# Performance work log

Measured on AMD Instinct MI355X. Metric: run time of the kernel, lower is better.

## Reference

```python
import jax, jax.numpy as jnp
import numpy as np

B, S, D, H, V, C = 4, 2048, 1024, 16, 32000, 10
FFN_DIM = 2 * D
HD = D // H
SCALE = float(np.sqrt(HD))


def _posenc(seq, d):
    pos = jnp.arange(seq, dtype=jnp.float32)[:, None]
    div = jnp.exp(jnp.arange(0, d, 2, dtype=jnp.float32) * (-np.log(10000.0) / d))
    pe = jnp.zeros((seq, d), dtype=jnp.float32)
    pe = pe.at[:, 0::2].set(jnp.sin(pos * div))
    pe = pe.at[:, 1::2].set(jnp.cos(pos * div))
    return pe


def _layernorm(x, g, b, eps=1e-5):
    mu = jnp.mean(x, axis=-1, keepdims=True)
    var = jnp.mean(jnp.square(x - mu), axis=-1, keepdims=True)
    return (x - mu) * jax.lax.rsqrt(var + eps) * g + b


def setup_inputs() -> dict:
    key = jax.random.key(0)
    ks = jax.random.split(key, 10)
    x_ids = jax.random.randint(ks[0], (B, S), 0, V, dtype=jnp.int64 if jax.config.jax_enable_x64 else jnp.int32)
    mask = jnp.ones((B, S), dtype=jnp.int32)
    emb = (jax.random.normal(ks[1], (V, D), jnp.float32) * 0.02).at[0].set(0.0)  # padding_idx=0
    qkv_w = jax.random.normal(ks[2], (3 * D, D), jnp.float32) * 0.02
    fc_w = jax.random.normal(ks[3], (D, D), jnp.float32) * 0.02
    fc_b = jnp.zeros((D,), jnp.float32)
    ln1_g = jnp.ones((D,), jnp.float32); ln1_b = jnp.zeros((D,), jnp.float32)
    ffn_w1 = jax.random.normal(ks[4], (FFN_DIM, D), jnp.float32) * 0.02
    ffn_b1 = jnp.zeros((FFN_DIM,), jnp.float32)
    ffn_w2 = jax.random.normal(ks[5], (D, FFN_DIM), jnp.float32) * 0.02
    ffn_b2 = jnp.zeros((D,), jnp.float32)
    ln2_g = jnp.ones((D,), jnp.float32); ln2_b = jnp.zeros((D,), jnp.float32)
    pr_w1 = jax.random.normal(ks[6], (D, D), jnp.float32) * 0.02
    pr_b1 = jnp.zeros((D,), jnp.float32)
    pr_w2 = jax.random.normal(ks[7], (C, D), jnp.float32) * 0.02
    pr_b2 = jnp.zeros((C,), jnp.float32)
    return dict(x_ids=x_ids, mask=mask, emb=emb, qkv_w=qkv_w, fc_w=fc_w, fc_b=fc_b,
                ln1_g=ln1_g, ln1_b=ln1_b, ffn_w1=ffn_w1, ffn_b1=ffn_b1,
                ffn_w2=ffn_w2, ffn_b2=ffn_b2, ln2_g=ln2_g, ln2_b=ln2_b,
                pr_w1=pr_w1, pr_b1=pr_b1, pr_w2=pr_w2, pr_b2=pr_b2)


def reference(x_ids, mask, emb, qkv_w, fc_w, fc_b, ln1_g, ln1_b,
              ffn_w1, ffn_b1, ffn_w2, ffn_b2, ln2_g, ln2_b,
              pr_w1, pr_b1, pr_w2, pr_b2):
    # embedding + absolute positional encoding
    x = emb[x_ids] + _posenc(S, D)  # [B,S,D]
    residual = x
    # multi-head attention (dropout is identity at eval)
    qkv = jnp.einsum('bsd,ed->bse', x, qkv_w)  # [B,S,3D]
    q, k, v = jnp.split(qkv, 3, axis=-1)
    q = q.reshape(B, S, H, HD)
    k = k.reshape(B, S, H, HD)
    v = v.reshape(B, S, H, HD)
    attn = jnp.einsum('bqhd,bkhd->bhqk', q, k) / SCALE  # [B,H,S,S]
    attn = jnp.where(mask[:, None, None, :] == 0, -jnp.inf, attn)
    attn = jax.nn.softmax(attn, axis=-1)
    o = jnp.einsum('bhqk,bkhd->bqhd', attn, v).reshape(B, S, D)
    o = jnp.einsum('bsd,ed->bse', o, fc_w) + fc_b
    x = _layernorm(o + residual, ln1_g, ln1_b)
    # FFN block (residual + LayerNorm inside)
    h = jax.nn.gelu(jnp.einsum('bsd,fd->bsf', x, ffn_w1) + ffn_b1, approximate=False)
    h = jnp.einsum('bsf,df->bsd', h, ffn_w2) + ffn_b2
    x = _layernorm(h + x, ln2_g, ln2_b)
    # masked max-pool over sequence
    x = jnp.where(mask[:, :, None] == 0, -jnp.inf, x).max(axis=1)  # [B,D]
    # prediction head
    h = jax.nn.gelu(x @ pr_w1.T + pr_b1, approximate=False)
    logits = h @ pr_w2.T + pr_b2  # [B,C]
    return logits
```

## Files before the change

kernel.cpp:

```cpp
#include <hip/hip_runtime.h>
#include <math.h>

#define B_   4
#define S_   2048
#define D_   1024
#define H_   16
#define HD_  64
#define C_   10
#define FFN_ 2048
#define M_   (B_ * S_)
#define D3_  (3 * D_)

typedef unsigned short u16;
typedef __bf16 bf16x8 __attribute__((ext_vector_type(8)));
typedef float  f32x4  __attribute__((ext_vector_type(4)));

#define EXPSCL 0.18033688011112042f

__device__ __forceinline__ u16 f2bf(float f) {
  union { float f; unsigned u; } x; x.f = f;
  unsigned r = x.u + 0x7fffu + ((x.u >> 16) & 1u);
  return (u16)(r >> 16);
}
__device__ __forceinline__ unsigned cvtpk(float lo, float hi) {
  unsigned r;
  asm("v_cvt_pk_bf16_f32 %0, %1, %2" : "=v"(r) : "v"(lo), "v"(hi));
  return r;
}
__device__ __forceinline__ float gelu_f(float x) {
  return 0.5f * x * (1.f + erff(x * 0.70710678118654752440f));
}
__device__ __forceinline__ void gload_lds16(const void* g, void* l) {
  __builtin_amdgcn_global_load_lds(
      (const __attribute__((address_space(1))) unsigned int*)g,
      (__attribute__((address_space(3))) unsigned int*)l, 16, 0, 0);
}
__device__ __forceinline__ bf16x8 ldsfrag(const u16* buf, int rowbase, int fr, int kb) {
  return *(const bf16x8*)&buf[(rowbase + fr) * 64 + ((kb ^ (fr & 7)) << 3)];
}

#define CV0 786432
#define CV1 262144
#define CV2 524288
#define CV3 524288
__global__ __launch_bounds__(256) void cvt4_kernel(const float* __restrict__ s0,
                                                   const float* __restrict__ s1,
                                                   const float* __restrict__ s2,
                                                   const float* __restrict__ s3,
                                                   u16* __restrict__ d0,
                                                   u16* __restrict__ d1,
                                                   u16* __restrict__ d2,
                                                   u16* __restrict__ d3) {
  int v = blockIdx.x * 256 + threadIdx.x;
  const float* s; u16* d;
  if (v < CV0) { s = s0; d = d0; }
  else if (v < CV0 + CV1) { s = s1; d = d1; v -= CV0; }
  else if (v < CV0 + CV1 + CV2) { s = s2; d = d2; v -= CV0 + CV1; }
  else { s = s3; d = d3; v -= CV0 + CV1 + CV2; }
  const int i = v * 4;
  f32x4 x = *(const f32x4*)&s[i];
  ushort4 o;
  o.x = f2bf(x[0]); o.y = f2bf(x[1]); o.z = f2bf(x[2]); o.w = f2bf(x[3]);
  *(ushort4*)&d[i] = o;
}

__global__ __launch_bounds__(256) void embed_kernel(const int* __restrict__ ids,
                                                    const float* __restrict__ emb,
                                                    float* __restrict__ resid,
                                                    u16* __restrict__ xb) {
  const int m  = blockIdx.x;
  const int s  = m & (S_ - 1);
  const int id = ids[m];
  const int d0 = threadIdx.x * 4;
#pragma unroll
  for (int k = 0; k < 4; ++k) {
    const int d   = d0 + k;
    const float e = emb[(size_t)id * D_ + d];
    const float fr  = expf((float)(d & ~1) * (-9.210340371976184f / 1024.0f));
    const float ang = (float)s * fr;
    const float pe  = (d & 1) ? cosf(ang) : sinf(ang);
    const float v   = e + pe;
    resid[(size_t)m * D_ + d] = v;
    xb[(size_t)m * D_ + d]    = f2bf(v);
  }
}

template <int BIAS, int GELU, int OUTBF, int QSCALE>
__global__ __launch_bounds__(256) void gemm_bt(const u16* __restrict__ A,
                                               const u16* __restrict__ W,
                                               const float* __restrict__ bias,
                                               float* __restrict__ outf,
                                               u16* __restrict__ outb,
                                               int M, int N, int K) {
  __shared__ u16 As[128 * 64];
  __shared__ u16 Bs[128 * 64];
  const int tid  = threadIdx.x;
  const int lane = tid & 63;
  const int w    = tid >> 6;
  const int bx   = blockIdx.x, by = blockIdx.y;
  const int l3   = lane >> 3;
  const int sb   = (lane & 7) ^ l3;
  const u16* Ag0 = A + (size_t)(by * 128 + w * 32 + l3) * K + sb * 8;
  const u16* Wg0 = W + (size_t)(bx * 128 + w * 32 + l3) * K + sb * 8;

  f32x4 acc[4][4] = {};
  const int wr  = (w & 1) * 64;
  const int wc  = (w >> 1) * 64;
  const int fr  = lane & 15;
  const int fq  = lane >> 4;

  for (int kt = 0; kt < K; kt += 64) {
#pragma unroll
    for (int c = 0; c < 4; ++c) {
      gload_lds16(Ag0 + (size_t)(c * 8) * K + kt, &As[(w * 32 + c * 8) * 64]);
      gload_lds16(Wg0 + (size_t)(c * 8) * K + kt, &Bs[(w * 32 + c * 8) * 64]);
    }
    __syncthreads();
#pragma unroll
    for (int ks = 0; ks < 2; ++ks) {
      const int kb = ks * 4 + fq;
      bf16x8 af[4], bfr[4];
#pragma unroll
      for (int i = 0; i < 4; ++i) af[i] = ldsfrag(As, wr + i * 16, fr, kb);
#pragma unroll
      for (int j = 0; j < 4; ++j) bfr[j] = ldsfrag(Bs, wc + j * 16, fr, kb);
#pragma unroll
      for (int i = 0; i < 4; ++i)
#pragma unroll
        for (int j = 0; j < 4; ++j)
          acc[i][j] = __builtin_amdgcn_mfma_f32_16x16x32_bf16(bfr[j], af[i], acc[i][j], 0, 0, 0);
    }
    __syncthreads();
  }

  const float qs = (QSCALE && bx < 8) ? EXPSCL : 1.f;
#pragma unroll
  for (int i = 0; i < 4; ++i) {
    const int m = by * 128 + wr + i * 16 + fr;
#pragma unroll
    for (int j = 0; j < 4; ++j) {
      const int nb = bx * 128 + wc + j * 16 + fq * 4;
      f32x4 v = acc[i][j];
      if (BIAS) v += *(const f32x4*)&bias[nb];
      if (GELU) {
        v[0] = gelu_f(v[0]); v[1] = gelu_f(v[1]);
        v[2] = gelu_f(v[2]); v[3] = gelu_f(v[3]);
      }
      if (QSCALE) v *= qs;
      if (OUTBF) {
        ushort4 pk;
        pk.x = f2bf(v[0]); pk.y = f2bf(v[1]); pk.z = f2bf(v[2]); pk.w = f2bf(v[3]);
        *(ushort4*)&outb[(size_t)m * N + nb] = pk;
      } else {
        *(f32x4*)&outf[(size_t)m * N + nb] = v;
      }
    }
  }
}

__global__ __launch_bounds__(256) void vtrans_kernel(const u16* __restrict__ qkv,
                                                     u16* __restrict__ vt) {
  __shared__ u16 t[64 * 65];
  const int tid = threadIdx.x;
  const int st = blockIdx.x, h = blockIdx.y, b = blockIdx.z;
  {
    const int r = tid & 63, cg = tid >> 6;
    const u16* src = qkv + (size_t)(b * S_ + st * 64 + r) * D3_ + 2 * D_ + h * 64 + cg * 16;
    union { uint4 q; u16 s[8]; } a, c;
    a.q = *(const uint4*)src;
    c.q = *(const uint4*)(src + 8);
    u16* dl = &t[r * 65 + cg * 16];
#pragma unroll
    for (int k = 0; k < 8; ++k) { dl[k] = a.s[k]; dl[8 + k] = c.s[k]; }
  }
  __syncthreads();
  const int d = tid >> 2, sq = tid & 3;
  union { uint4 q[2]; u16 s[16]; } o;
#pragma unroll
  for (int k = 0; k < 16; ++k) o.s[k] = t[(sq * 16 + k) * 65 + d];
  u16* dst = vt + ((size_t)((b * H_ + h) * 64 + d)) * S_ + st * 64 + sq * 16;
  *(uint4*)dst = o.q[0];
  *(uint4*)(dst + 8) = o.q[1];
}

__global__ __launch_bounds__(256) void attn_mfma_kernel(const u16* __restrict__ qkv,
                                                        const u16* __restrict__ vt,
                                                        const int* __restrict__ mask,
                                                        u16* __restrict__ attno) {
  __shared__ u16 Qs[128 * 64];
  __shared__ u16 Ks[64 * 64];
  __shared__ u16 Vts[64 * 64];
  __shared__ u16 Ps[4][16 * 64];
  int* allv_p = (int*)&Ps[0][0];
  const int tid = threadIdx.x, lane = tid & 63, w = tid >> 6;
  const int qt = blockIdx.x, h = blockIdx.y, b = blockIdx.z;
  const int l3 = lane >> 3;
  const int sb = (lane & 7) ^ l3;
  const int fr = lane & 15, fq = lane >> 4;

  {
    const u16* qbase = qkv + (size_t)(b * S_ + qt * 128 + w * 32) * D3_ + h * 64 + sb * 8;
#pragma unroll
    for (int c = 0; c < 4; ++c)
      gload_lds16(qbase + (size_t)(c * 8 + l3) * D3_, &Qs[(w * 32 + c * 8) * 64]);
  }
  if (tid == 0) *allv_p = 1;
  __syncthreads();
  {
    int mv = 1;
#pragma unroll
    for (int s0 = 0; s0 < 8; ++s0) mv &= (mask[b * S_ + s0 * 256 + tid] != 0);
    if (__ballot(mv != 0) != ~0ull) {
      if (lane == 0) atomicAnd(allv_p, 0);
    }
  }
  __syncthreads();
  const bool ALLV = (*allv_p != 0);

  float l_st[2] = {0.f, 0.f};
  f32x4 ot[4][2] = {};
  u16* PsW = Ps[w];

  for (int kt = 0; kt < S_ / 64; ++kt) {
    __syncthreads();
    {
      const u16* kbase = qkv + (size_t)(b * S_ + kt * 64 + w * 16) * D3_ + D_ + h * 64 + sb * 8;
      gload_lds16(kbase + (size_t)l3 * D3_, &Ks[(w * 16) * 64]);
      gload_lds16(kbase + (size_t)(8 + l3) * D3_, &Ks[(w * 16 + 8) * 64]);
      const u16* vbase = vt + ((size_t)((b * H_ + h) * 64 + w * 16)) * S_ + kt * 64 + sb * 8;
      gload_lds16(vbase + (size_t)l3 * S_, &Vts[(w * 16) * 64]);
      gload_lds16(vbase + (size_t)(8 + l3) * S_, &Vts[(w * 16 + 8) * 64]);
    }
    __syncthreads();

    f32x4 sf[4][2] = {};
#pragma unroll
    for (int ks = 0; ks < 2; ++ks) {
      const int kb = ks * 4 + fq;
      bf16x8 qf0 = ldsfrag(Qs, w * 32, fr, kb);
      bf16x8 qf1 = ldsfrag(Qs, w * 32 + 16, fr, kb);
      __builtin_amdgcn_s_setprio(1);
#pragma unroll
      for (int r4 = 0; r4 < 4; ++r4) {
        bf16x8 kf = ldsfrag(Ks, r4 * 16, fr, kb);
        sf[r4][0] = __builtin_amdgcn_mfma_f32_16x16x32_bf16(kf, qf0, sf[r4][0], 0, 0, 0);
        sf[r4][1] = __builtin_amdgcn_mfma_f32_16x16x32_bf16(kf, qf1, sf[r4][1], 0, 0, 0);
      }
      __builtin_amdgcn_s_setprio(0);
    }
    if (!ALLV) {
#pragma unroll
      for (int r4 = 0; r4 < 4; ++r4) {
        const int4 mm = *(const int4*)&mask[b * S_ + kt * 64 + r4 * 16 + fq * 4];
        f32x4 vb;
        vb[0] = mm.x ? 0.f : -1e30f;
        vb[1] = mm.y ? 0.f : -1e30f;
        vb[2] = mm.z ? 0.f : -1e30f;
        vb[3] = mm.w ? 0.f : -1e30f;
        sf[r4][0] += vb;
        sf[r4][1] += vb;
      }
    }

#pragma unroll
    for (int i = 0; i < 2; ++i) {
      u16* pw = PsW + fr * 64;
      float sum = l_st[i];
#pragma unroll
      for (int r4 = 0; r4 < 4; ++r4) {
        const float p0 = __builtin_exp2f(sf[r4][i][0]);
        const float p1 = __builtin_exp2f(sf[r4][i][1]);
        const float p2 = __builtin_exp2f(sf[r4][i][2]);
        const float p3 = __builtin_exp2f(sf[r4][i][3]);
        sum += (p0 + p1) + (p2 + p3);
        const int bk0 = 2 * r4 + (fq >> 1);
        const int off = ((bk0 ^ (fr & 7)) << 3) + ((fq & 1) << 2);
        uint2 pk; pk.x = cvtpk(p0, p1); pk.y = cvtpk(p2, p3);
        *(uint2*)&pw[off] = pk;
      }
      l_st[i] = sum;
      asm volatile("s_waitcnt lgkmcnt(0)" ::: "memory");

      bf16x8 pf0 = ldsfrag(PsW, 0, fr, fq);
      bf16x8 pf1 = ldsfrag(PsW, 0, fr, 4 + fq);
      __builtin_amdgcn_s_setprio(1);
#pragma unroll
      for (int db = 0; db < 4; ++db) {
        bf16x8 vf0 = ldsfrag(Vts, db * 16, fr, fq);
        bf16x8 vf1 = ldsfrag(Vts, db * 16, fr, 4 + fq);
        ot[db][i] = __builtin_amdgcn_mfma_f32_16x16x32_bf16(vf0, pf0, ot[db][i], 0, 0, 0);
        ot[db][i] = __builtin_amdgcn_mfma_f32_16x16x32_bf16(vf1, pf1, ot[db][i], 0, 0, 0);
      }
      __builtin_amdgcn_s_setprio(0);
    }
  }

#pragma unroll
  for (int i = 0; i < 2; ++i) {
    float l = l_st[i];
    l += __shfl_xor(l, 16);
    l += __shfl_xor(l, 32);
    const float inv = (l > 0.f) ? 1.f / l : 0.f;
    const int qrow = qt * 128 + w * 32 + i * 16 + fr;
    u16* dst = attno + (size_t)(b * S_ + qrow) * D_ + h * 64 + fq * 4;
#pragma unroll
    for (int db = 0; db < 4; ++db) {
      ushort4 pk;
      pk.x = f2bf(ot[db][i][0] * inv);
      pk.y = f2bf(ot[db][i][1] * inv);
      pk.z = f2bf(ot[db][i][2] * inv);
      pk.w = f2bf(ot[db][i][3] * inv);
      *(ushort4*)&dst[db * 16] = pk;
    }
  }
}

template <int WRITEB>
__global__ __launch_bounds__(256) void ln_kernel(const float* __restrict__ a,
                                                 const float* __restrict__ res,
                                                 const float* __restrict__ g,
                                                 const float* __restrict__ be,
                                                 float* __restrict__ outf,
                                                 u16* __restrict__ outb) {
  const int row = blockIdx.x, tid = threadIdx.x;
  const int lane = tid & 63, w = tid >> 6;
  const size_t base = (size_t)row * D_ + tid * 4;
  const f32x4 va = *(const f32x4*)(a + base);
  const f32x4 vr = *(const f32x4*)(res + base);
  const f32x4 v  = va + vr;
  float s = v[0] + v[1] + v[2] + v[3];
#pragma unroll
  for (int o = 32; o > 0; o >>= 1) s += __shfl_xor(s, o);
  __shared__ float red[8];
  if (lane == 0) red[w] = s;
  __syncthreads();
  const float mu = (red[0] + red[1] + red[2] + red[3]) * (1.f / D_);
  const f32x4 d = v - mu;
  float s2 = d[0] * d[0] + d[1] * d[1] + d[2] * d[2] + d[3] * d[3];
#pragma unroll
  for (int o = 32; o > 0; o >>= 1) s2 += __shfl_xor(s2, o);
  if (lane == 0) red[4 + w] = s2;
  __syncthreads();
  const float var = (red[4] + red[5] + red[6] + red[7]) * (1.f / D_);
  const float rs = rsqrtf(var + 1e-5f);
  f32x4 y;
#pragma unroll
  for (int k = 0; k < 4; ++k) {
    const int ch = tid * 4 + k;
    y[k] = d[k] * rs * g[ch] + be[ch];
  }
  *(f32x4*)&outf[base] = y;
  if (WRITEB) {
    ushort4 pk;
    pk.x = f2bf(y[0]); pk.y = f2bf(y[1]); pk.z = f2bf(y[2]); pk.w = f2bf(y[3]);
    *(ushort4*)&outb[base] = pk;
  }
}

__global__ __launch_bounds__(256) void pool_part_kernel(const float* __restrict__ x,
                                                        const int* __restrict__ mask,
                                                        float* __restrict__ part) {
  const int b = blockIdx.y, ch = blockIdx.x;
  const int d0 = threadIdx.x * 4;
  f32x4 acc = {-INFINITY, -INFINITY, -INFINITY, -INFINITY};
  for (int ss = 0; ss < 64; ++ss) {
    const int s = ch * 64 + ss;
    if (mask[b * S_ + s] != 0) {
      const f32x4 v = *(const f32x4*)&x[(size_t)(b * S_ + s) * D_ + d0];
      acc[0] = fmaxf(acc[0], v[0]);
      acc[1] = fmaxf(acc[1], v[1]);
      acc[2] = fmaxf(acc[2], v[2]);
      acc[3] = fmaxf(acc[3], v[3]);
    }
  }
  *(f32x4*)&part[(size_t)(b * 32 + ch) * D_ + d0] = acc;
}
__global__ __launch_bounds__(256) void pool_final_kernel(const float* __restrict__ part,
                                                         float* __restrict__ pooled) {
  const int b = blockIdx.x;
  const int d0 = threadIdx.x * 4;
  f32x4 acc = {-INFINITY, -INFINITY, -INFINITY, -INFINITY};
  for (int ch = 0; ch < 32; ++ch) {
    const f32x4 v = *(const f32x4*)&part[(size_t)(b * 32 + ch) * D_ + d0];
    acc[0] = fmaxf(acc[0], v[0]);
    acc[1] = fmaxf(acc[1], v[1]);
    acc[2] = fmaxf(acc[2], v[2]);
    acc[3] = fmaxf(acc[3], v[3]);
  }
  *(f32x4*)&pooled[(size_t)b * D_ + d0] = acc;
}

__global__ __launch_bounds__(256) void head1_kernel(const float* __restrict__ pooled,
                                                    const float* __restrict__ w,
                                                    const float* __restrict__ bias,
                                                    float* __restrict__ hh) {
  const int lane = threadIdx.x & 63;
  const int gw = blockIdx.x * 4 + (threadIdx.x >> 6);
  const int b = gw >> 10, n = gw & 1023;
  const float* p  = pooled + b * 1024;
  const float* wr = w + (size_t)n * 1024;
  float s = 0.f;
  for (int d = lane; d < 1024; d += 64) s += p[d] * wr[d];
#pragma unroll
  for (int off = 32; off > 0; off >>= 1) s += __shfl_xor(s, off);
  if (lane == 0) hh[b * 1024 + n] = gelu_f(s + bias[n]);
}
__global__ __launch_bounds__(256) void head2_kernel(const float* __restrict__ hh,
                                                    const float* __restrict__ w,
                                                    const float* __restrict__ bias,
                                                    float* __restrict__ out) {
  const int lane = threadIdx.x & 63;
  const int gw = blockIdx.x * 4 + (threadIdx.x >> 6);
  const int b = gw / 10, c = gw % 10;
  const float* p  = hh + b * 1024;
  const float* wr = w + (size_t)c * 1024;
  float s = 0.f;
  for (int d = lane; d < 1024; d += 64) s += p[d] * wr[d];
#pragma unroll
  for (int off = 32; off > 0; off >>= 1) s += __shfl_xor(s, off);
  if (lane == 0) out[b * 10 + c] = s + bias[c];
}

#define OFF_RESID  0UL
#define OFF_F1     33554432UL
#define OFF_XB     67108864UL
#define OFF_QKVB   83886080UL
#define OFF_ATTNO  134217728UL
#define OFF_WQKV   150994944UL
#define OFF_WFC    157286400UL
#define OFF_WF1    159383552UL
#define OFF_WF2    163577856UL
#define OFF_PART   167772160UL
#define OFF_POOLED 168296448UL
#define OFF_HH     168312832UL

extern "C" void kernel_launch(void* const* d_in, const int* in_sizes, int n_in,
                              void* d_out, int out_size, void* d_ws, size_t ws_size,
                              hipStream_t stream) {
  const int*   x_ids  = (const int*)d_in[0];
  const int*   mask   = (const int*)d_in[1];
  const float* emb    = (const float*)d_in[2];
  const float* qkv_w  = (const float*)d_in[3];
  const float* fc_w   = (const float*)d_in[4];
  const float* fc_b   = (const float*)d_in[5];
  const float* ln1_g  = (const float*)d_in[6];
  const float* ln1_b  = (const float*)d_in[7];
  const float* ffn_w1 = (const float*)d_in[8];
  const float* ffn_b1 = (const float*)d_in[9];
  const float* ffn_w2 = (const float*)d_in[10];
  const float* ffn_b2 = (const float*)d_in[11];
  const float* ln2_g  = (const float*)d_in[12];
  const float* ln2_b  = (const float*)d_in[13];
  const float* pr_w1  = (const float*)d_in[14];
  const float* pr_b1  = (const float*)d_in[15];
  const float* pr_w2  = (const float*)d_in[16];
  const float* pr_b2  = (const float*)d_in[17];
  float* out = (float*)d_out;
  char* ws = (char*)d_ws;

  float* resid  = (float*)(ws + OFF_RESID);
  float* f1     = (float*)(ws + OFF_F1);
  u16*   vtb    = (u16*)(ws + OFF_F1);
  u16*   xb     = (u16*)(ws + OFF_XB);
  u16*   qkvb   = (u16*)(ws + OFF_QKVB);
  u16*   hb     = (u16*)(ws + OFF_QKVB);
  u16*   attnob = (u16*)(ws + OFF_ATTNO);
  u16*   wqkvb  = (u16*)(ws + OFF_WQKV);
  u16*   wfcb   = (u16*)(ws + OFF_WFC);
  u16*   wf1b   = (u16*)(ws + OFF_WF1);
  u16*   wf2b   = (u16*)(ws + OFF_WF2);
  float* part   = (float*)(ws + OFF_PART);
  float* pooled = (float*)(ws + OFF_POOLED);
  float* hh     = (float*)(ws + OFF_HH);

  cvt4_kernel<<<8192, 256, 0, stream>>>(qkv_w, fc_w, ffn_w1, ffn_w2,
                                        wqkvb, wfcb, wf1b, wf2b);

  embed_kernel<<<M_, 256, 0, stream>>>(x_ids, emb, resid, xb);

  gemm_bt<0, 0, 1, 1><<<dim3(D3_ / 128, M_ / 128), 256, 0, stream>>>(
      xb, wqkvb, nullptr, nullptr, qkvb, M_, D3_, D_);

  vtrans_kernel<<<dim3(S_ / 64, H_, B_), 256, 0, stream>>>(qkvb, vtb);

  attn_mfma_kernel<<<dim3(S_ / 128, H_, B_), 256, 0, stream>>>(qkvb, vtb, mask, attnob);

  gemm_bt<1, 0, 0, 0><<<dim3(D_ / 128, M_ / 128), 256, 0, stream>>>(
      attnob, wfcb, fc_b, f1, nullptr, M_, D_, D_);

  ln_kernel<1><<<M_, 256, 0, stream>>>(f1, resid, ln1_g, ln1_b, resid, xb);

  gemm_bt<1, 1, 1, 0><<<dim3(FFN_ / 128, M_ / 128), 256, 0, stream>>>(
      xb, wf1b, ffn_b1, nullptr, hb, M_, FFN_, D_);

  gemm_bt<1, 0, 0, 0><<<dim3(D_ / 128, M_ / 128), 256, 0, stream>>>(
      hb, wf2b, ffn_b2, f1, nullptr, M_, D_, FFN_);

  ln_kernel<0><<<M_, 256, 0, stream>>>(f1, resid, ln2_g, ln2_b, f1, nullptr);

  pool_part_kernel<<<dim3(32, B_), 256, 0, stream>>>(f1, mask, part);
  pool_final_kernel<<<B_, 256, 0, stream>>>(part, pooled);

  head1_kernel<<<1024, 256, 0, stream>>>(pooled, pr_w1, pr_b1, hh);
  head2_kernel<<<10, 256, 0, stream>>>(hh, pr_w2, pr_b2, out);
}
```

Baseline: 638.1 us.

## Double-buffer K/V tiles in LDS and keep Q fragments in registers

The attention kernel now prefetches the next K/V tile into a second LDS buffer while the current tile is computed, so only one barrier is needed per iteration. Q fragments are loaded once into registers, and the Q staging area is reused for the K/V buffers. This hides global-to-LDS latency and removes repeated Q LDS reads. The cost is more VGPR pressure, and correctness depends on the async LDS loads being complete at each barrier.

```diff
diff --git a/kernel.cpp b/kernel.cpp
--- a/kernel.cpp
+++ b/kernel.cpp
@@ -187,9 +187,7 @@
                                                         const u16* __restrict__ vt,
                                                         const int* __restrict__ mask,
                                                         u16* __restrict__ attno) {
-  __shared__ u16 Qs[128 * 64];
-  __shared__ u16 Ks[64 * 64];
-  __shared__ u16 Vts[64 * 64];
+  __shared__ u16 KV[2][2][64 * 64];
   __shared__ u16 Ps[4][16 * 64];
   int* allv_p = (int*)&Ps[0][0];
   const int tid = threadIdx.x, lane = tid & 63, w = tid >> 6;
@@ -197,15 +195,24 @@
   const int l3 = lane >> 3;
   const int sb = (lane & 7) ^ l3;
   const int fr = lane & 15, fq = lane >> 4;
+  u16* KVflat = &KV[0][0][0];
 
   {
     const u16* qbase = qkv + (size_t)(b * S_ + qt * 128 + w * 32) * D3_ + h * 64 + sb * 8;
 #pragma unroll
     for (int c = 0; c < 4; ++c)
-      gload_lds16(qbase + (size_t)(c * 8 + l3) * D3_, &Qs[(w * 32 + c * 8) * 64]);
+      gload_lds16(qbase + (size_t)(c * 8 + l3) * D3_, &KVflat[(w * 32 + c * 8) * 64]);
   }
   if (tid == 0) *allv_p = 1;
   __syncthreads();
+
+  bf16x8 qf[2][2];
+#pragma unroll
+  for (int ks = 0; ks < 2; ++ks)
+#pragma unroll
+    for (int i = 0; i < 2; ++i)
+      qf[ks][i] = ldsfrag(KVflat, w * 32 + i * 16, fr, ks * 4 + fq);
+
   {
     int mv = 1;
 #pragma unroll
@@ -217,34 +224,41 @@
   __syncthreads();
   const bool ALLV = (*allv_p != 0);
 
+  const u16* kb_g = qkv + (size_t)(b * S_ + w * 16 + l3) * D3_ + D_ + h * 64 + sb * 8;
+  const u16* vb_g = vt + ((size_t)((b * H_ + h) * 64 + w * 16 + l3)) * S_ + sb * 8;
+
+#define STAGE_KV(t, buf)                                                      \
+  {                                                                           \
+    const u16* kk = kb_g + (size_t)(t) * (64 * D3_);                          \
+    const u16* vv = vb_g + (t) * 64;                                          \
+    gload_lds16(kk, &KV[buf][0][(w * 16) * 64]);                              \
+    gload_lds16(kk + (size_t)8 * D3_, &KV[buf][0][(w * 16 + 8) * 64]);        \
+    gload_lds16(vv, &KV[buf][1][(w * 16) * 64]);                              \
+    gload_lds16(vv + (size_t)8 * S_, &KV[buf][1][(w * 16 + 8) * 64]);         \
+  }
+
+  STAGE_KV(0, 0);
+
   float l_st[2] = {0.f, 0.f};
   f32x4 ot[4][2] = {};
   u16* PsW = Ps[w];
 
   for (int kt = 0; kt < S_ / 64; ++kt) {
     __syncthreads();
-    {
-      const u16* kbase = qkv + (size_t)(b * S_ + kt * 64 + w * 16) * D3_ + D_ + h * 64 + sb * 8;
-      gload_lds16(kbase + (size_t)l3 * D3_, &Ks[(w * 16) * 64]);
-      gload_lds16(kbase + (size_t)(8 + l3) * D3_, &Ks[(w * 16 + 8) * 64]);
-      const u16* vbase = vt + ((size_t)((b * H_ + h) * 64 + w * 16)) * S_ + kt * 64 + sb * 8;
-      gload_lds16(vbase + (size_t)l3 * S_, &Vts[(w * 16) * 64]);
-      gload_lds16(vbase + (size_t)(8 + l3) * S_, &Vts[(w * 16 + 8) * 64]);
-    }
-    __syncthreads();
+    if (kt + 1 < S_ / 64) STAGE_KV(kt + 1, (kt + 1) & 1);
+    const u16* Kc = KV[kt & 1][0];
+    const u16* Vc = KV[kt & 1][1];
 
     f32x4 sf[4][2] = {};
 #pragma unroll
     for (int ks = 0; ks < 2; ++ks) {
       const int kb = ks * 4 + fq;
-      bf16x8 qf0 = ldsfrag(Qs, w * 32, fr, kb);
-      bf16x8 qf1 = ldsfrag(Qs, w * 32 + 16, fr, kb);
       __builtin_amdgcn_s_setprio(1);
 #pragma unroll
       for (int r4 = 0; r4 < 4; ++r4) {
-        bf16x8 kf = ldsfrag(Ks, r4 * 16, fr, kb);
-        sf[r4][0] = __builtin_amdgcn_mfma_f32_16x16x32_bf16(kf, qf0, sf[r4][0], 0, 0, 0);
-        sf[r4][1] = __builtin_amdgcn_mfma_f32_16x16x32_bf16(kf, qf1, sf[r4][1], 0, 0, 0);
+        bf16x8 kf = ldsfrag(Kc, r4 * 16, fr, kb);
+        sf[r4][0] = __builtin_amdgcn_mfma_f32_16x16x32_bf16(kf, qf[ks][0], sf[r4][0], 0, 0, 0);
+        sf[r4][1] = __builtin_amdgcn_mfma_f32_16x16x32_bf16(kf, qf[ks][1], sf[r4][1], 0, 0, 0);
       }
       __builtin_amdgcn_s_setprio(0);
     }
@@ -286,14 +300,15 @@
       __builtin_amdgcn_s_setprio(1);
 #pragma unroll
       for (int db = 0; db < 4; ++db) {
-        bf16x8 vf0 = ldsfrag(Vts, db * 16, fr, fq);
-        bf16x8 vf1 = ldsfrag(Vts, db * 16, fr, 4 + fq);
+        bf16x8 vf0 = ldsfrag(Vc, db * 16, fr, fq);
+        bf16x8 vf1 = ldsfrag(Vc, db * 16, fr, 4 + fq);
         ot[db][i] = __builtin_amdgcn_mfma_f32_16x16x32_bf16(vf0, pf0, ot[db][i], 0, 0, 0);
         ot[db][i] = __builtin_amdgcn_mfma_f32_16x16x32_bf16(vf1, pf1, ot[db][i], 0, 0, 0);
       }
       __builtin_amdgcn_s_setprio(0);
     }
   }
+#undef STAGE_KV
 
 #pragma unroll
   for (int i = 0; i < 2; ++i) {
```

After: 680.4 us. 6.6% more time.

## Hold Q fragments in registers and share V fragments across both query halves

Applied to the files above, without the earlier changes.

Q fragments are loaded from LDS once into registers before the key loop, so they are no longer reloaded every tile. The Q staging buffer is aliased onto an enlarged P buffer, with each wave now owning a 32-row P tile. The P·V step is restructured so each V fragment read from LDS feeds both 16-row query halves, halving V LDS reads. The mask all-valid check uses vectorized per-wave loads and a ballot instead of a shared atomic flag, and the per-tile barrier moves to the end of the loop. This raises register pressure, which may lower occupancy.

```diff
diff --git a/kernel.cpp b/kernel.cpp
--- a/kernel.cpp
+++ b/kernel.cpp
@@ -187,42 +187,51 @@
                                                         const u16* __restrict__ vt,
                                                         const int* __restrict__ mask,
                                                         u16* __restrict__ attno) {
-  __shared__ u16 Qs[128 * 64];
   __shared__ u16 Ks[64 * 64];
   __shared__ u16 Vts[64 * 64];
-  __shared__ u16 Ps[4][16 * 64];
-  int* allv_p = (int*)&Ps[0][0];
+  __shared__ u16 Ps[4][32 * 64];
   const int tid = threadIdx.x, lane = tid & 63, w = tid >> 6;
   const int qt = blockIdx.x, h = blockIdx.y, b = blockIdx.z;
   const int l3 = lane >> 3;
   const int sb = (lane & 7) ^ l3;
   const int fr = lane & 15, fq = lane >> 4;
+  u16* PsFlat = &Ps[0][0];
 
   {
     const u16* qbase = qkv + (size_t)(b * S_ + qt * 128 + w * 32) * D3_ + h * 64 + sb * 8;
 #pragma unroll
     for (int c = 0; c < 4; ++c)
-      gload_lds16(qbase + (size_t)(c * 8 + l3) * D3_, &Qs[(w * 32 + c * 8) * 64]);
-  }
-  if (tid == 0) *allv_p = 1;
+      gload_lds16(qbase + (size_t)(c * 8 + l3) * D3_, &PsFlat[(w * 32 + c * 8) * 64]);
+  }
+
+  bool ALLV;
+  {
+    const int4* mp = (const int4*)&mask[b * S_];
+    int mv = 1;
+#pragma unroll
+    for (int t = 0; t < 8; ++t) {
+      const int4 m4 = mp[t * 64 + lane];
+      mv &= (m4.x != 0) & (m4.y != 0) & (m4.z != 0) & (m4.w != 0);
+    }
+    ALLV = (__ballot(mv != 0) == ~0ull);
+  }
+
   __syncthreads();
-  {
-    int mv = 1;
-#pragma unroll
-    for (int s0 = 0; s0 < 8; ++s0) mv &= (mask[b * S_ + s0 * 256 + tid] != 0);
-    if (__ballot(mv != 0) != ~0ull) {
-      if (lane == 0) atomicAnd(allv_p, 0);
-    }
-  }
+
+  bf16x8 qf[2][2];
+#pragma unroll
+  for (int ks = 0; ks < 2; ++ks)
+#pragma unroll
+    for (int i = 0; i < 2; ++i)
+      qf[ks][i] = ldsfrag(PsFlat, w * 32 + i * 16, fr, ks * 4 + fq);
+
   __syncthreads();
-  const bool ALLV = (*allv_p != 0);
 
   float l_st[2] = {0.f, 0.f};
   f32x4 ot[4][2] = {};
   u16* PsW = Ps[w];
 
   for (int kt = 0; kt < S_ / 64; ++kt) {
-    __syncthreads();
     {
       const u16* kbase = qkv + (size_t)(b * S_ + kt * 64 + w * 16) * D3_ + D_ + h * 64 + sb * 8;
       gload_lds16(kbase + (size_t)l3 * D3_, &Ks[(w * 16) * 64]);
@@ -237,14 +246,12 @@
 #pragma unroll
     for (int ks = 0; ks < 2; ++ks) {
       const int kb = ks * 4 + fq;
-      bf16x8 qf0 = ldsfrag(Qs, w * 32, fr, kb);
-      bf16x8 qf1 = ldsfrag(Qs, w * 32 + 16, fr, kb);
       __builtin_amdgcn_s_setprio(1);
 #pragma unroll
       for (int r4 = 0; r4 < 4; ++r4) {
         bf16x8 kf = ldsfrag(Ks, r4 * 16, fr, kb);
-        sf[r4][0] = __builtin_amdgcn_mfma_f32_16x16x32_bf16(kf, qf0, sf[r4][0], 0, 0, 0);
-        sf[r4][1] = __builtin_amdgcn_mfma_f32_16x16x32_bf16(kf, qf1, sf[r4][1], 0, 0, 0);
+        sf[r4][0] = __builtin_amdgcn_mfma_f32_16x16x32_bf16(kf, qf[ks][0], sf[r4][0], 0, 0, 0);
+        sf[r4][1] = __builtin_amdgcn_mfma_f32_16x16x32_bf16(kf, qf[ks][1], sf[r4][1], 0, 0, 0);
       }
       __builtin_amdgcn_s_setprio(0);
     }
@@ -264,7 +271,8 @@
 
 #pragma unroll
     for (int i = 0; i < 2; ++i) {
-      u16* pw = PsW + fr * 64;
+      const int prow = i * 16 + fr;
+      u16* pw = PsW + prow * 64;
       float sum = l_st[i];
 #pragma unroll
       for (int r4 = 0; r4 < 4; ++r4) {
@@ -274,25 +282,29 @@
         const float p3 = __builtin_exp2f(sf[r4][i][3]);
         sum += (p0 + p1) + (p2 + p3);
         const int bk0 = 2 * r4 + (fq >> 1);
-        const int off = ((bk0 ^ (fr & 7)) << 3) + ((fq & 1) << 2);
+        const int off = ((bk0 ^ (prow & 7)) << 3) + ((fq & 1) << 2);
         uint2 pk; pk.x = cvtpk(p0, p1); pk.y = cvtpk(p2, p3);
         *(uint2*)&pw[off] = pk;
       }
       l_st[i] = sum;
-      asm volatile("s_waitcnt lgkmcnt(0)" ::: "memory");
-
-      bf16x8 pf0 = ldsfrag(PsW, 0, fr, fq);
-      bf16x8 pf1 = ldsfrag(PsW, 0, fr, 4 + fq);
+    }
+    asm volatile("s_waitcnt lgkmcnt(0)" ::: "memory");
+
+#pragma unroll
+    for (int ks = 0; ks < 2; ++ks) {
+      const int kb = ks * 4 + fq;
+      bf16x8 pf0 = ldsfrag(PsW, 0, fr, kb);
+      bf16x8 pf1 = ldsfrag(PsW, 16, fr, kb);
       __builtin_amdgcn_s_setprio(1);
 #pragma unroll
       for (int db = 0; db < 4; ++db) {
-        bf16x8 vf0 = ldsfrag(Vts, db * 16, fr, fq);
-        bf16x8 vf1 = ldsfrag(Vts, db * 16, fr, 4 + fq);
-        ot[db][i] = __builtin_amdgcn_mfma_f32_16x16x32_bf16(vf0, pf0, ot[db][i], 0, 0, 0);
-        ot[db][i] = __builtin_amdgcn_mfma_f32_16x16x32_bf16(vf1, pf1, ot[db][i], 0, 0, 0);
+        bf16x8 vf = ldsfrag(Vts, db * 16, fr, kb);
+        ot[db][0] = __builtin_amdgcn_mfma_f32_16x16x32_bf16(vf, pf0, ot[db][0], 0, 0, 0);
+        ot[db][1] = __builtin_amdgcn_mfma_f32_16x16x32_bf16(vf, pf1, ot[db][1], 0, 0, 0);
       }
       __builtin_amdgcn_s_setprio(0);
     }
+    __syncthreads();
   }
 
 #pragma unroll
```

New measurement: 656.3 us. 1.03x slower.
